# Optimization experiments

Measured on AMD Instinct MI355X. Metric: run time of the kernel, lower is better.

## Reference

```python
import jax, jax.numpy as jnp
import numpy as np

B, T, I, H, O = 128, 512, 512, 2048, 512

def setup_inputs() -> dict:
    key = jax.random.key(0)
    ks = jax.random.split(key, 10)
    s = lambda fan_in: 1.0 / np.sqrt(fan_in)
    return {
        "x": jax.random.normal(ks[0], (B, T, I), dtype=jnp.float32),
        "dt": jnp.zeros((1,), dtype=jnp.float32),            # torch init: Tensor([0])
        "a": jnp.ones((1,), dtype=jnp.float32),              # torch init: Tensor([1])
        "enc_w": jax.random.uniform(ks[1], (H, I), jnp.float32, -s(I), s(I)),
        "enc_b": jax.random.uniform(ks[2], (H,), jnp.float32, -s(I), s(I)),
        "rec_w": jax.random.uniform(ks[3], (H, H), jnp.float32, -s(H), s(H)),
        "rec_b": jax.random.uniform(ks[4], (H,), jnp.float32, -s(H), s(H)),
        "dec_w": jax.random.uniform(ks[5], (O, H), jnp.float32, -s(H), s(H)),
        "dec_b": jax.random.uniform(ks[6], (O,), jnp.float32, -s(H), s(H)),
        "hi_w": jax.random.uniform(ks[7], (H, 1), jnp.float32, -1.0, 1.0),
        "hi_b": jax.random.uniform(ks[8], (H,), jnp.float32, -1.0, 1.0),
    }

def reference(x, dt, a, enc_w, enc_b, rec_w, rec_b, dec_w, dec_b, hi_w, hi_b):
    # x: [B, T, I] -> time-major [T, B, I]
    xt = jnp.transpose(x, (1, 0, 2))
    sdt = jax.nn.sigmoid(dt[0])          # scalar gate
    av = a[0]
    # hidden_init(ones(B,1)) = hi_w[:,0] + hi_b, broadcast over batch
    h0 = jnp.broadcast_to(hi_w[:, 0] + hi_b, (x.shape[0], hi_b.shape[0]))
    # precompute encoder projection for all timesteps: [T, B, H]
    enc = jnp.einsum('tbi,hi->tbh', xt, enc_w) + enc_b

    def step(h, e_t):
        h = (1.0 - sdt) * h + sdt * jnp.tanh(e_t + av * (h @ rec_w.T + rec_b))
        y = h @ dec_w.T + dec_b
        return h, y

    hidden, output = jax.lax.scan(step, h0, enc)
    return output, hidden
```

## Files before the change

kernel.cpp:

```cpp
#include <hip/hip_runtime.h>
#include <hip/hip_bf16.h>
#include <cmath>

#define Bb 128
#define Tt 512
#define Ii 512
#define Hh 2048
#define Oo 512
#define REC_GRID 256

typedef __bf16 bf16_t;
typedef __bf16 bf16x8 __attribute__((ext_vector_type(8)));
typedef __bf16 bf16x4 __attribute__((ext_vector_type(4)));
typedef float  f32x4_t __attribute__((ext_vector_type(4)));
typedef unsigned u32;

static __device__ __forceinline__ bf16_t to_b(float v){ return (bf16_t)v; }
static __device__ __forceinline__ float  b2f(unsigned short u){ unsigned x = ((unsigned)u)<<16; return __builtin_bit_cast(float, x); }
static __device__ __forceinline__ unsigned short f2bbits(float v){ return __builtin_bit_cast(unsigned short, to_b(v)); }

static __device__ __forceinline__ void gl_lds16(const void* g, void* l){
  __builtin_amdgcn_global_load_lds((const __attribute__((address_space(1))) void*)g,
                                   (__attribute__((address_space(3))) void*)l, 16, 0, 0);
}

#define REP4(M) M(0)M(1)M(2)M(3)

__global__ __launch_bounds__(256) void k_f2b(bf16_t* __restrict__ dst, const float* __restrict__ src){
  size_t i = ((size_t)blockIdx.x*256 + threadIdx.x)*4;
  float4 v = *(const float4*)(src + i);
  bf16x4 o; o[0]=to_b(v.x); o[1]=to_b(v.y); o[2]=to_b(v.z); o[3]=to_b(v.w);
  *(bf16x4*)(dst + i) = o;
}

__global__ __launch_bounds__(256) void k_init_h0(const float* __restrict__ hi_w, const float* __restrict__ hi_b,
                                                 bf16_t* __restrict__ h0b){
  int i = blockIdx.x*256 + threadIdx.x;
  bf16_t vb = to_b(hi_w[i] + hi_b[i]);
  for (int b=0;b<Bb;++b) h0b[(size_t)b*Hh + i] = vb;
}

__global__ __launch_bounds__(256) void k_convert_x(const float* __restrict__ x, bf16_t* __restrict__ x_tm){
  size_t idx = ((size_t)blockIdx.x*256 + threadIdx.x)*8;
  int    i0  = (int)(idx % Ii);
  size_t m   = idx / Ii;
  int    t   = (int)(m / Bb), b = (int)(m % Bb);
  const float* s = x + ((size_t)b*Tt + t)*Ii + i0;
  float4 v0 = *(const float4*)s, v1 = *(const float4*)(s+4);
  bf16x8 o;
  o[0]=to_b(v0.x); o[1]=to_b(v0.y); o[2]=to_b(v0.z); o[3]=to_b(v0.w);
  o[4]=to_b(v1.x); o[5]=to_b(v1.y); o[6]=to_b(v1.z); o[7]=to_b(v1.w);
  *(bf16x8*)(x_tm + idx) = o;
}

template<int ROWS, int KB>
static __device__ __forceinline__ void stage(const bf16_t* __restrict__ g, long ld, long row0, int k0,
                                             char* __restrict__ ldsT){
  constexpr int SLOTS = KB/8;
  constexpr int PT    = ROWS*SLOTS/256;
  #pragma unroll
  for (int j=0;j<PT;++j){
    int c    = threadIdx.x + 256*j;
    int row  = c / SLOTS, slot = c % SLOTS;
    uint4 v  = *(const uint4*)(g + (row0+row)*ld + k0 + slot*8);
    *(uint4*)(ldsT + row*(KB*2) + ((slot*16) ^ ((row&7)<<4))) = v;
  }
}

template<int KB>
static __device__ __forceinline__ bf16x8 frag(const char* __restrict__ ldsT, int row, int kk, int lane){
  int kbyte = kk*64 + ((lane>>4)<<4);
  return *(const bf16x8*)(ldsT + row*(KB*2) + (kbyte ^ ((row&7)<<4)));
}

template<int EPI>
__global__ __launch_bounds__(256) void gemm128(const bf16_t* __restrict__ A, long lda,
                                               const bf16_t* __restrict__ Bw, long ldb,
                                               const float* __restrict__ bias,
                                               void* __restrict__ Cout, long ldc, int K){
  constexpr int TM=128, TN=128, KB=64;
  __shared__ char lds[(TM+TN)*KB*2];
  char* ldsA = lds;
  char* ldsB = lds + TM*KB*2;
  long m0 = (long)blockIdx.x * TM;
  long n0 = (long)blockIdx.y * TN;
  int w = threadIdx.x >> 6, lane = threadIdx.x & 63;
  int wm = w >> 1, wn = w & 1;
  f32x4_t acc[4][4] = {};
  for (int k0=0;k0<K;k0+=KB){
    __syncthreads();
    stage<TM,KB>(A,  lda, m0, k0, ldsA);
    stage<TN,KB>(Bw, ldb, n0, k0, ldsB);
    __syncthreads();
    #pragma unroll
    for (int kk=0;kk<KB/32;++kk){
      bf16x8 af[4], bfv[4];
      #pragma unroll
      for (int f=0;f<4;++f){ int r = wm*64 + f*16 + (lane&15); af[f]  = frag<KB>(ldsA, r, kk, lane); }
      #pragma unroll
      for (int f=0;f<4;++f){ int r = wn*64 + f*16 + (lane&15); bfv[f] = frag<KB>(ldsB, r, kk, lane); }
      #pragma unroll
      for (int i=0;i<4;++i)
        #pragma unroll
        for (int j=0;j<4;++j)
          acc[i][j] = __builtin_amdgcn_mfma_f32_16x16x32_bf16(af[i], bfv[j], acc[i][j], 0,0,0);
    }
  }
  #pragma unroll
  for (int i=0;i<4;++i)
    #pragma unroll
    for (int j=0;j<4;++j)
      #pragma unroll
      for (int e=0;e<4;++e){
        long row = m0 + wm*64 + i*16 + ((lane>>4)<<2) + e;
        long col = n0 + wn*64 + j*16 + (lane&15);
        float v = acc[i][j][e] + bias[col];
        if (EPI==0) ((bf16_t*)Cout)[row*ldc + col] = to_b(v);
        else        ((float*) Cout)[row*ldc + col] = v;
      }
}

__global__ __launch_bounds__(1024, 1) void rec_persist(
    const bf16_t* __restrict__ h0b, const bf16_t* __restrict__ W,
    bf16_t* __restrict__ EH, float* __restrict__ hfinal,
    const float* __restrict__ rec_b, const float* __restrict__ hi_w, const float* __restrict__ hi_b,
    const float* __restrict__ dtp, const float* __restrict__ ap,
    unsigned* __restrict__ flags)
{
  __shared__ char lds[65536 + 65536 + 4352];
  char*  hbuf = lds;
  float* redf = (float*)(lds + 65536);
  float* xbf  = (float*)(lds + 131072);

  const int bid = blockIdx.x;
  const int g   = bid & 7;
  const int n   = bid >> 3;
  const int m0  = g * 16;
  const int n0  = n * 64;
  unsigned* gflags = flags + g*32*16;
  const int tid = threadIdx.x, w = tid >> 6, lane = tid & 63;
  const int l15 = lane & 15, w4 = w*4;

  #define WDCL(i) bf16x8 wa##i, wb##i, wc##i, wd##i;
  REP4(WDCL)
  #undef WDCL
  #pragma unroll 1
  for (int p = 0; p < 2; ++p){
    __syncthreads();
    for (int it = 0; it < 8; ++it){
      int cid = it*1024 + tid;
      int lc  = cid & 63, kk = (cid >> 6) & 63, cgl = cid >> 12;
      uint4 v = *(const uint4*)(W + (size_t)(n0 + p*32 + cgl*16 + (lc&15))*Hh + kk*32 + ((lc>>4)<<3));
      *(uint4*)(lds + (size_t)cid*16) = v;
    }
    __syncthreads();
    if (p == 0){
      #define WRD(i) \
        wa##i = *(const bf16x8*)(lds + (size_t)((     w4 + (i))*64 + lane)*16); \
        wb##i = *(const bf16x8*)(lds + (size_t)((64 + w4 + (i))*64 + lane)*16);
      REP4(WRD)
      #undef WRD
    } else {
      #define WRD(i) \
        wc##i = *(const bf16x8*)(lds + (size_t)((     w4 + (i))*64 + lane)*16); \
        wd##i = *(const bf16x8*)(lds + (size_t)((64 + w4 + (i))*64 + lane)*16);
      REP4(WRD)
      #undef WRD
    }
  }
  __syncthreads();

  const float s  = 1.f/(1.f + __expf(-dtp[0]));
  const float av = ap[0];
  const int   cg_o = w & 3, eo = w >> 2;
  const int   batch = m0 + l15;
  const int   col_l = cg_o*16 + ((lane >> 4) << 2) + eo;
  const int   hcol  = n0 + col_l;
  const int   pos   = l15*65 + col_l;
  const float rbv = rec_b[hcol];
  float hm = hi_w[hcol] + hi_b[hcol];

  const size_t vsrc_off = (size_t)(m0 + l15)*Hh + ((lane>>4)<<3);
  const int co_b = m0 + (tid >> 5);
  const int co_c = n0 + (tid & 31)*2;
  const unsigned* fp = gflags + (w*2 + (lane & 1))*16;

  for (int t = 0; t < Tt; ++t){
    const bf16_t* Asrc = (t==0) ? h0b : (EH + (size_t)(t-1)*(Bb*Hh));
    bf16_t* EHt = EH + (size_t)t*(Bb*Hh);

    u32 ecv = 0;
    if (tid < 512)
      ecv = __hip_atomic_load((const u32*)(EHt + (size_t)co_b*Hh + co_c),
                              __ATOMIC_RELAXED, __HIP_MEMORY_SCOPE_AGENT);

    if (t){
      unsigned tt = (unsigned)t;
      for (;;){
        unsigned v = __hip_atomic_load(fp, __ATOMIC_RELAXED, __HIP_MEMORY_SCOPE_AGENT);
        if (__all((int)(v >= tt))) break;
        __builtin_amdgcn_s_sleep(2);
      }
    }

    {
      const bf16_t* src = Asrc + vsrc_off;
      #pragma unroll
      for (int i = 0; i < 4; ++i)
        gl_lds16(src + (w4 + i)*32, hbuf + (size_t)(w4 + i)*1024);
    }
    asm volatile("s_waitcnt vmcnt(0)" ::: "memory");

    f32x4_t acc0 = {0.f,0.f,0.f,0.f}, acc1 = acc0, acc2 = acc0, acc3 = acc0;
    #define KS(i) { \
      bf16x8 hv = *(const bf16x8*)(hbuf + (size_t)(w4 + (i))*1024 + (size_t)lane*16); \
      acc0 = __builtin_amdgcn_mfma_f32_16x16x32_bf16(wa##i, hv, acc0, 0,0,0); \
      acc1 = __builtin_amdgcn_mfma_f32_16x16x32_bf16(wb##i, hv, acc1, 0,0,0); \
      acc2 = __builtin_amdgcn_mfma_f32_16x16x32_bf16(wc##i, hv, acc2, 0,0,0); \
      acc3 = __builtin_amdgcn_mfma_f32_16x16x32_bf16(wd##i, hv, acc3, 0,0,0); }
    REP4(KS)
    #undef KS

    #pragma unroll
    for (int e=0;e<4;++e){
      redf[(w*16 +  0 + e)*64 + lane] = acc0[e];
      redf[(w*16 +  4 + e)*64 + lane] = acc1[e];
      redf[(w*16 +  8 + e)*64 + lane] = acc2[e];
      redf[(w*16 + 12 + e)*64 + lane] = acc3[e];
    }
    if (tid < 512){
      xbf[(tid>>5)*65 + (tid&31)*2    ] = b2f((unsigned short)(ecv & 0xffffu));
      xbf[(tid>>5)*65 + (tid&31)*2 + 1] = b2f((unsigned short)(ecv >> 16));
    }
    __syncthreads();

    float fa = 0.f;
    #pragma unroll
    for (int q=0;q<16;++q) fa += redf[(q*16 + cg_o*4 + eo)*64 + lane];

    {
      float enc = xbf[pos];
      float pre = enc + av*(fa + rbv);
      float th  = 1.f - 2.f/(__expf(2.f*pre) + 1.f);
      hm = (1.f - s)*hm + s*th;
      xbf[pos] = hm;
    }
    __syncthreads();

    if (tid < 512){
      float h0f = xbf[(tid>>5)*65 + (tid&31)*2];
      float h1f = xbf[(tid>>5)*65 + (tid&31)*2 + 1];
      u32 ov = (u32)f2bbits(h0f) | ((u32)f2bbits(h1f) << 16);
      __hip_atomic_store((u32*)(EHt + (size_t)co_b*Hh + co_c), ov,
                         __ATOMIC_RELAXED, __HIP_MEMORY_SCOPE_AGENT);
    }
    __syncthreads();
    if (tid == 0)
      __hip_atomic_store(gflags + n*16, (unsigned)(t+1),
                         __ATOMIC_RELAXED, __HIP_MEMORY_SCOPE_AGENT);
  }

  hfinal[(size_t)batch*Hh + hcol] = hm;
}

extern "C" void kernel_launch(void* const* d_in, const int* in_sizes, int n_in,
                              void* d_out, int out_size, void* d_ws, size_t ws_size,
                              hipStream_t stream){
  const float* x     = (const float*)d_in[0];
  const float* dt    = (const float*)d_in[1];
  const float* a     = (const float*)d_in[2];
  const float* enc_w = (const float*)d_in[3];
  const float* enc_b = (const float*)d_in[4];
  const float* rec_w = (const float*)d_in[5];
  const float* rec_b = (const float*)d_in[6];
  const float* dec_w = (const float*)d_in[7];
  const float* dec_b = (const float*)d_in[8];
  const float* hi_w  = (const float*)d_in[9];
  const float* hi_b  = (const float*)d_in[10];
  float* out = (float*)d_out;

  char* ws = (char*)d_ws;
  size_t off = 0;
  auto carve = [&](size_t bytes)->char*{ char* p = ws + off; off += (bytes + 255) & ~(size_t)255; return p; };
  bf16_t* x_tm   = (bf16_t*)carve((size_t)Tt*Bb*Ii*2);
  bf16_t* EH     = (bf16_t*)carve((size_t)Tt*Bb*Hh*2);
  bf16_t* h0b    = (bf16_t*)carve((size_t)Bb*Hh*2);
  bf16_t* enc_wb = (bf16_t*)carve((size_t)Hh*Ii*2);
  bf16_t* rec_wb = (bf16_t*)carve((size_t)Hh*Hh*2);
  bf16_t* dec_wb = (bf16_t*)carve((size_t)Oo*Hh*2);
  unsigned* flags = (unsigned*)carve(8*32*16*4);
  if (off > ws_size) return;

  hipMemsetAsync(flags, 0, 8*32*16*4, stream);

  k_f2b<<<(Hh*Ii)/1024, 256, 0, stream>>>(enc_wb, enc_w);
  k_f2b<<<(Hh*Hh)/1024, 256, 0, stream>>>(rec_wb, rec_w);
  k_f2b<<<(Oo*Hh)/1024, 256, 0, stream>>>(dec_wb, dec_w);
  k_init_h0<<<Hh/256, 256, 0, stream>>>(hi_w, hi_b, h0b);
  k_convert_x<<<((size_t)Tt*Bb*Ii/8)/256, 256, 0, stream>>>(x, x_tm);

  gemm128<0><<<dim3((Tt*Bb)/128, Hh/128), 256, 0, stream>>>(x_tm, Ii, enc_wb, Ii, enc_b, EH, Hh, Ii);

  {
    float* hfinal = out + (size_t)Tt*Bb*Oo;
    void* args[] = { (void*)&h0b, (void*)&rec_wb, (void*)&EH, (void*)&hfinal,
                     (void*)&rec_b, (void*)&hi_w, (void*)&hi_b, (void*)&dt, (void*)&a,
                     (void*)&flags };
    hipLaunchCooperativeKernel((const void*)rec_persist, dim3(REC_GRID), dim3(1024), args, 0, stream);
  }

  gemm128<1><<<dim3((Tt*Bb)/128, Oo/128), 256, 0, stream>>>(EH, Hh, dec_wb, Hh, dec_b, out, Oo, Hh);
}
```

Before: 2.406 ms.

## Split recurrent step into two batch halves with double-buffered h loads

Each block's 16 batch rows are split into two 8-row halves, each with its own set of progress flags and its own LDS buffer for h. While one half is being computed, the global-to-LDS load of the other half's previous hidden state is already in flight, so cross-block synchronisation latency overlaps with MFMA work. The waves are also re-partitioned to cover 8 k-chunks and 2 column groups each, with a two-stage LDS reduction in place of the old 16-way sum. In exchange, MFMAs still run over all 16 rows and only half the results are kept, so matrix work per step doubles. The change also adds more barriers and doubles the flag array.

```diff
diff --git a/kernel.cpp b/kernel.cpp
--- a/kernel.cpp
+++ b/kernel.cpp
@@ -24,7 +24,7 @@
                                    (__attribute__((address_space(3))) void*)l, 16, 0, 0);
 }
 
-#define REP4(M) M(0)M(1)M(2)M(3)
+#define REP8(M) M(0)M(1)M(2)M(3)M(4)M(5)M(6)M(7)
 
 __global__ __launch_bounds__(256) void k_f2b(bf16_t* __restrict__ dst, const float* __restrict__ src){
   size_t i = ((size_t)blockIdx.x*256 + threadIdx.x)*4;
@@ -127,44 +127,38 @@
     const float* __restrict__ dtp, const float* __restrict__ ap,
     unsigned* __restrict__ flags)
 {
-  __shared__ char lds[65536 + 65536 + 4352];
-  char*  hbuf = lds;
-  float* redf = (float*)(lds + 65536);
-  float* xbf  = (float*)(lds + 131072);
+  __shared__ char lds[65536 + 65536 + 16384 + 4352];
+  char*  hbufA = lds;
+  char*  hbufB = lds + 65536;
+  float* redf  = (float*)(lds + 131072);
+  float* xbf   = (float*)(lds + 147456);
 
   const int bid = blockIdx.x;
-  const int g   = bid & 7;
+  const int p   = bid & 7;
   const int n   = bid >> 3;
-  const int m0  = g * 16;
+  const int m0  = p * 16;
   const int n0  = n * 64;
-  unsigned* gflags = flags + g*32*16;
   const int tid = threadIdx.x, w = tid >> 6, lane = tid & 63;
   const int l15 = lane & 15, w4 = w*4;
-
-  #define WDCL(i) bf16x8 wa##i, wb##i, wc##i, wd##i;
-  REP4(WDCL)
-  #undef WDCL
+  const int ch = w & 1, ko = w >> 1, ko8 = ko*8;
+
+  bf16x8 wE0,wE1,wE2,wE3,wE4,wE5,wE6,wE7;
+  bf16x8 wO0,wO1,wO2,wO3,wO4,wO5,wO6,wO7;
   #pragma unroll 1
-  for (int p = 0; p < 2; ++p){
+  for (int p2 = 0; p2 < 2; ++p2){
     __syncthreads();
     for (int it = 0; it < 8; ++it){
       int cid = it*1024 + tid;
       int lc  = cid & 63, kk = (cid >> 6) & 63, cgl = cid >> 12;
-      uint4 v = *(const uint4*)(W + (size_t)(n0 + p*32 + cgl*16 + (lc&15))*Hh + kk*32 + ((lc>>4)<<3));
+      uint4 v = *(const uint4*)(W + (size_t)(n0 + p2*32 + cgl*16 + (lc&15))*Hh + kk*32 + ((lc>>4)<<3));
       *(uint4*)(lds + (size_t)cid*16) = v;
     }
     __syncthreads();
-    if (p == 0){
+    if (p2 == ch){
       #define WRD(i) \
-        wa##i = *(const bf16x8*)(lds + (size_t)((     w4 + (i))*64 + lane)*16); \
-        wb##i = *(const bf16x8*)(lds + (size_t)((64 + w4 + (i))*64 + lane)*16);
-      REP4(WRD)
-      #undef WRD
-    } else {
-      #define WRD(i) \
-        wc##i = *(const bf16x8*)(lds + (size_t)((     w4 + (i))*64 + lane)*16); \
-        wd##i = *(const bf16x8*)(lds + (size_t)((64 + w4 + (i))*64 + lane)*16);
-      REP4(WRD)
+        wE##i = *(const bf16x8*)(lds + (size_t)((     ko8 + (i))*64 + lane)*16); \
+        wO##i = *(const bf16x8*)(lds + (size_t)((64 + ko8 + (i))*64 + lane)*16);
+      REP8(WRD)
       #undef WRD
     }
   }
@@ -179,14 +173,28 @@
   const int   pos   = l15*65 + col_l;
   const float rbv = rec_b[hcol];
   float hm = hi_w[hcol] + hi_b[hcol];
+  const bool validA = (l15 < 8), validB = (l15 >= 8);
 
   const size_t vsrc_off = (size_t)(m0 + l15)*Hh + ((lane>>4)<<3);
   const int co_b = m0 + (tid >> 5);
   const int co_c = n0 + (tid & 31)*2;
-  const unsigned* fp = gflags + (w*2 + (lane & 1))*16;
+  const unsigned* fpA = flags + (((2*p  )*32) + ko*4 + (lane & 3))*16;
+  const unsigned* fpB = flags + (((2*p+1)*32) + ko*4 + (lane & 3))*16;
+  unsigned* flA = flags + ((2*p  )*32 + n)*16;
+  unsigned* flB = flags + ((2*p+1)*32 + n)*16;
+
+  auto volley = [&](const bf16_t* Asrc, char* hb){
+    const bf16_t* src = Asrc + vsrc_off;
+    #pragma unroll
+    for (int i = 0; i < 4; ++i)
+      gl_lds16(src + (w4 + i)*32, hb + (size_t)(w4 + i)*1024);
+  };
+
+  volley(h0b, hbufA);
+  __syncthreads();
 
   for (int t = 0; t < Tt; ++t){
-    const bf16_t* Asrc = (t==0) ? h0b : (EH + (size_t)(t-1)*(Bb*Hh));
+    const bf16_t* Aprev = (t==0) ? h0b : (EH + (size_t)(t-1)*(Bb*Hh));
     bf16_t* EHt = EH + (size_t)t*(Bb*Hh);
 
     u32 ecv = 0;
@@ -197,67 +205,131 @@
     if (t){
       unsigned tt = (unsigned)t;
       for (;;){
-        unsigned v = __hip_atomic_load(fp, __ATOMIC_RELAXED, __HIP_MEMORY_SCOPE_AGENT);
+        unsigned v = __hip_atomic_load(fpB, __ATOMIC_RELAXED, __HIP_MEMORY_SCOPE_AGENT);
         if (__all((int)(v >= tt))) break;
         __builtin_amdgcn_s_sleep(2);
       }
     }
+    volley(Aprev, hbufB);
 
     {
-      const bf16_t* src = Asrc + vsrc_off;
-      #pragma unroll
-      for (int i = 0; i < 4; ++i)
-        gl_lds16(src + (w4 + i)*32, hbuf + (size_t)(w4 + i)*1024);
-    }
-    asm volatile("s_waitcnt vmcnt(0)" ::: "memory");
-
-    f32x4_t acc0 = {0.f,0.f,0.f,0.f}, acc1 = acc0, acc2 = acc0, acc3 = acc0;
-    #define KS(i) { \
-      bf16x8 hv = *(const bf16x8*)(hbuf + (size_t)(w4 + (i))*1024 + (size_t)lane*16); \
-      acc0 = __builtin_amdgcn_mfma_f32_16x16x32_bf16(wa##i, hv, acc0, 0,0,0); \
-      acc1 = __builtin_amdgcn_mfma_f32_16x16x32_bf16(wb##i, hv, acc1, 0,0,0); \
-      acc2 = __builtin_amdgcn_mfma_f32_16x16x32_bf16(wc##i, hv, acc2, 0,0,0); \
-      acc3 = __builtin_amdgcn_mfma_f32_16x16x32_bf16(wd##i, hv, acc3, 0,0,0); }
-    REP4(KS)
-    #undef KS
-
-    #pragma unroll
-    for (int e=0;e<4;++e){
-      redf[(w*16 +  0 + e)*64 + lane] = acc0[e];
-      redf[(w*16 +  4 + e)*64 + lane] = acc1[e];
-      redf[(w*16 +  8 + e)*64 + lane] = acc2[e];
-      redf[(w*16 + 12 + e)*64 + lane] = acc3[e];
-    }
-    if (tid < 512){
-      xbf[(tid>>5)*65 + (tid&31)*2    ] = b2f((unsigned short)(ecv & 0xffffu));
-      xbf[(tid>>5)*65 + (tid&31)*2 + 1] = b2f((unsigned short)(ecv >> 16));
-    }
-    __syncthreads();
-
-    float fa = 0.f;
-    #pragma unroll
-    for (int q=0;q<16;++q) fa += redf[(q*16 + cg_o*4 + eo)*64 + lane];
+      f32x4_t aE = {0.f,0.f,0.f,0.f}, aO = aE;
+      #define KS(i) { \
+        bf16x8 hv = *(const bf16x8*)(hbufA + (size_t)(ko8 + (i))*1024 + (size_t)lane*16); \
+        aE = __builtin_amdgcn_mfma_f32_16x16x32_bf16(wE##i, hv, aE, 0,0,0); \
+        aO = __builtin_amdgcn_mfma_f32_16x16x32_bf16(wO##i, hv, aO, 0,0,0); }
+      REP8(KS)
+      #undef KS
+      if (ko >= 4){
+        #pragma unroll
+        for (int e=0;e<4;++e){
+          redf[(((ko-4)*4 + ch*2    )*4 + e)*64 + lane] = aE[e];
+          redf[(((ko-4)*4 + ch*2 + 1)*4 + e)*64 + lane] = aO[e];
+        }
+      }
+      if (tid < 256){
+        xbf[(tid>>5)*65 + (tid&31)*2    ] = b2f((unsigned short)(ecv & 0xffffu));
+        xbf[(tid>>5)*65 + (tid&31)*2 + 1] = b2f((unsigned short)(ecv >> 16));
+      }
+      __syncthreads();
+      if (ko < 4){
+        #pragma unroll
+        for (int e=0;e<4;++e){
+          aE[e] += redf[((ko*4 + ch*2    )*4 + e)*64 + lane];
+          aO[e] += redf[((ko*4 + ch*2 + 1)*4 + e)*64 + lane];
+        }
+        #pragma unroll
+        for (int e=0;e<4;++e){
+          redf[((ko*4 + ch*2    )*4 + e)*64 + lane] = aE[e];
+          redf[((ko*4 + ch*2 + 1)*4 + e)*64 + lane] = aO[e];
+        }
+      }
+      __syncthreads();
+      float fa = 0.f;
+      #pragma unroll
+      for (int kp=0;kp<4;++kp) fa += redf[((kp*4 + cg_o)*4 + eo)*64 + lane];
+      {
+        float enc = xbf[pos];
+        float pre = enc + av*(fa + rbv);
+        float th  = 1.f - 2.f/(__expf(2.f*pre) + 1.f);
+        if (validA){ hm = (1.f - s)*hm + s*th; xbf[pos] = hm; }
+      }
+      __syncthreads();
+      if (tid < 256){
+        float h0f = xbf[(tid>>5)*65 + (tid&31)*2];
+        float h1f = xbf[(tid>>5)*65 + (tid&31)*2 + 1];
+        u32 ov = (u32)f2bbits(h0f) | ((u32)f2bbits(h1f) << 16);
+        __hip_atomic_store((u32*)(EHt + (size_t)co_b*Hh + co_c), ov,
+                           __ATOMIC_RELAXED, __HIP_MEMORY_SCOPE_AGENT);
+      }
+      __syncthreads();
+      if (tid == 0)
+        __hip_atomic_store(flA, (unsigned)(t+1), __ATOMIC_RELAXED, __HIP_MEMORY_SCOPE_AGENT);
+    }
 
     {
-      float enc = xbf[pos];
-      float pre = enc + av*(fa + rbv);
-      float th  = 1.f - 2.f/(__expf(2.f*pre) + 1.f);
-      hm = (1.f - s)*hm + s*th;
-      xbf[pos] = hm;
-    }
-    __syncthreads();
-
-    if (tid < 512){
-      float h0f = xbf[(tid>>5)*65 + (tid&31)*2];
-      float h1f = xbf[(tid>>5)*65 + (tid&31)*2 + 1];
-      u32 ov = (u32)f2bbits(h0f) | ((u32)f2bbits(h1f) << 16);
-      __hip_atomic_store((u32*)(EHt + (size_t)co_b*Hh + co_c), ov,
-                         __ATOMIC_RELAXED, __HIP_MEMORY_SCOPE_AGENT);
-    }
-    __syncthreads();
-    if (tid == 0)
-      __hip_atomic_store(gflags + n*16, (unsigned)(t+1),
-                         __ATOMIC_RELAXED, __HIP_MEMORY_SCOPE_AGENT);
+      f32x4_t aE = {0.f,0.f,0.f,0.f}, aO = aE;
+      #define KS(i) { \
+        bf16x8 hv = *(const bf16x8*)(hbufB + (size_t)(ko8 + (i))*1024 + (size_t)lane*16); \
+        aE = __builtin_amdgcn_mfma_f32_16x16x32_bf16(wE##i, hv, aE, 0,0,0); \
+        aO = __builtin_amdgcn_mfma_f32_16x16x32_bf16(wO##i, hv, aO, 0,0,0); }
+      REP8(KS)
+      #undef KS
+      if (ko >= 4){
+        #pragma unroll
+        for (int e=0;e<4;++e){
+          redf[(((ko-4)*4 + ch*2    )*4 + e)*64 + lane] = aE[e];
+          redf[(((ko-4)*4 + ch*2 + 1)*4 + e)*64 + lane] = aO[e];
+        }
+      }
+      if (tid >= 256 && tid < 512){
+        xbf[(tid>>5)*65 + (tid&31)*2    ] = b2f((unsigned short)(ecv & 0xffffu));
+        xbf[(tid>>5)*65 + (tid&31)*2 + 1] = b2f((unsigned short)(ecv >> 16));
+      }
+      __syncthreads();
+      if (ko < 4){
+        #pragma unroll
+        for (int e=0;e<4;++e){
+          aE[e] += redf[((ko*4 + ch*2    )*4 + e)*64 + lane];
+          aO[e] += redf[((ko*4 + ch*2 + 1)*4 + e)*64 + lane];
+        }
+        #pragma unroll
+        for (int e=0;e<4;++e){
+          redf[((ko*4 + ch*2    )*4 + e)*64 + lane] = aE[e];
+          redf[((ko*4 + ch*2 + 1)*4 + e)*64 + lane] = aO[e];
+        }
+      }
+      __syncthreads();
+      float fa = 0.f;
+      #pragma unroll
+      for (int kp=0;kp<4;++kp) fa += redf[((kp*4 + cg_o)*4 + eo)*64 + lane];
+      {
+        float enc = xbf[pos];
+        float pre = enc + av*(fa + rbv);
+        float th  = 1.f - 2.f/(__expf(2.f*pre) + 1.f);
+        if (validB){ hm = (1.f - s)*hm + s*th; xbf[pos] = hm; }
+      }
+      __syncthreads();
+      if (tid >= 256 && tid < 512){
+        float h0f = xbf[(tid>>5)*65 + (tid&31)*2];
+        float h1f = xbf[(tid>>5)*65 + (tid&31)*2 + 1];
+        u32 ov = (u32)f2bbits(h0f) | ((u32)f2bbits(h1f) << 16);
+        __hip_atomic_store((u32*)(EHt + (size_t)co_b*Hh + co_c), ov,
+                           __ATOMIC_RELAXED, __HIP_MEMORY_SCOPE_AGENT);
+      }
+      if (t+1 < Tt){
+        unsigned tt = (unsigned)(t+1);
+        for (;;){
+          unsigned v = __hip_atomic_load(fpA, __ATOMIC_RELAXED, __HIP_MEMORY_SCOPE_AGENT);
+          if (__all((int)(v >= tt))) break;
+          __builtin_amdgcn_s_sleep(2);
+        }
+        volley(EHt, hbufA);
+      }
+      __syncthreads();
+      if (tid == 0)
+        __hip_atomic_store(flB, (unsigned)(t+1), __ATOMIC_RELAXED, __HIP_MEMORY_SCOPE_AGENT);
+    }
   }
 
   hfinal[(size_t)batch*Hh + hcol] = hm;
@@ -288,10 +360,10 @@
   bf16_t* enc_wb = (bf16_t*)carve((size_t)Hh*Ii*2);
   bf16_t* rec_wb = (bf16_t*)carve((size_t)Hh*Hh*2);
   bf16_t* dec_wb = (bf16_t*)carve((size_t)Oo*Hh*2);
-  unsigned* flags = (unsigned*)carve(8*32*16*4);
+  unsigned* flags = (unsigned*)carve(16*32*16*4);
   if (off > ws_size) return;
 
-  hipMemsetAsync(flags, 0, 8*32*16*4, stream);
+  hipMemsetAsync(flags, 0, 16*32*16*4, stream);
 
   k_f2b<<<(Hh*Ii)/1024, 256, 0, stream>>>(enc_wb, enc_w);
   k_f2b<<<(Hh*Hh)/1024, 256, 0, stream>>>(rec_wb, rec_w);
```

Measured after the change: 4.211 ms. +75.0%, slower.

## Use per-wave flags and fuse elementwise update to cut recurrent step barriers

Applied to the files above, without the earlier changes.

The recurrent step's epilogue is restructured so that 8 waves each compute two hidden columns directly from the reduced partial sums and write them to global memory, removing the xbf staging buffer and two block barriers. Each wave then publishes its own progress flag instead of one flag per block, and consumers poll per-wave flags before loading the next h slice into LDS at the end of the step. This shortens the critical path of the 512 serial steps. In exchange the flag array is larger and each consumer polls more flags, which adds polling traffic.

```diff
diff --git a/kernel.cpp b/kernel.cpp
--- a/kernel.cpp
+++ b/kernel.cpp
@@ -127,17 +127,16 @@
     const float* __restrict__ dtp, const float* __restrict__ ap,
     unsigned* __restrict__ flags)
 {
-  __shared__ char lds[65536 + 65536 + 4352];
+  __shared__ char lds[131072];
   char*  hbuf = lds;
   float* redf = (float*)(lds + 65536);
-  float* xbf  = (float*)(lds + 131072);
 
   const int bid = blockIdx.x;
   const int g   = bid & 7;
   const int n   = bid >> 3;
   const int m0  = g * 16;
   const int n0  = n * 64;
-  unsigned* gflags = flags + g*32*16;
+  unsigned* gflags = flags + g*256*16;
   const int tid = threadIdx.x, w = tid >> 6, lane = tid & 63;
   const int l15 = lane & 15, w4 = w*4;
 
@@ -172,44 +171,36 @@
 
   const float s  = 1.f/(1.f + __expf(-dtp[0]));
   const float av = ap[0];
-  const int   cg_o = w & 3, eo = w >> 2;
+  const int   cg_o = w & 3, ep = (w >> 2) & 1;
   const int   batch = m0 + l15;
-  const int   col_l = cg_o*16 + ((lane >> 4) << 2) + eo;
-  const int   hcol  = n0 + col_l;
-  const int   pos   = l15*65 + col_l;
-  const float rbv = rec_b[hcol];
-  float hm = hi_w[hcol] + hi_b[hcol];
+  const int   c0    = cg_o*16 + ((lane >> 4) << 2) + ep*2;
+  const size_t eoff = (size_t)batch*Hh + n0 + c0;
+  float rb0 = 0.f, rb1 = 0.f, hm0 = 0.f, hm1 = 0.f;
+  if (w < 8){
+    rb0 = rec_b[n0 + c0];     rb1 = rec_b[n0 + c0 + 1];
+    hm0 = hi_w[n0 + c0] + hi_b[n0 + c0];
+    hm1 = hi_w[n0 + c0 + 1] + hi_b[n0 + c0 + 1];
+  }
 
   const size_t vsrc_off = (size_t)(m0 + l15)*Hh + ((lane>>4)<<3);
-  const int co_b = m0 + (tid >> 5);
-  const int co_c = n0 + (tid & 31)*2;
-  const unsigned* fp = gflags + (w*2 + (lane & 1))*16;
+  const unsigned* fp = gflags + ((w*2 + ((lane>>3)&1))*8 + (lane&7))*16;
+  unsigned* myflag = gflags + (n*8 + w)*16;
+
+  {
+    const bf16_t* src = h0b + vsrc_off;
+    #pragma unroll
+    for (int i = 0; i < 4; ++i)
+      gl_lds16(src + (w4 + i)*32, hbuf + (size_t)(w4 + i)*1024);
+  }
+  asm volatile("s_waitcnt vmcnt(0)" ::: "memory");
 
   for (int t = 0; t < Tt; ++t){
-    const bf16_t* Asrc = (t==0) ? h0b : (EH + (size_t)(t-1)*(Bb*Hh));
     bf16_t* EHt = EH + (size_t)t*(Bb*Hh);
 
     u32 ecv = 0;
-    if (tid < 512)
-      ecv = __hip_atomic_load((const u32*)(EHt + (size_t)co_b*Hh + co_c),
+    if (w < 8)
+      ecv = __hip_atomic_load((const u32*)(EHt + eoff),
                               __ATOMIC_RELAXED, __HIP_MEMORY_SCOPE_AGENT);
-
-    if (t){
-      unsigned tt = (unsigned)t;
-      for (;;){
-        unsigned v = __hip_atomic_load(fp, __ATOMIC_RELAXED, __HIP_MEMORY_SCOPE_AGENT);
-        if (__all((int)(v >= tt))) break;
-        __builtin_amdgcn_s_sleep(2);
-      }
-    }
-
-    {
-      const bf16_t* src = Asrc + vsrc_off;
-      #pragma unroll
-      for (int i = 0; i < 4; ++i)
-        gl_lds16(src + (w4 + i)*32, hbuf + (size_t)(w4 + i)*1024);
-    }
-    asm volatile("s_waitcnt vmcnt(0)" ::: "memory");
 
     f32x4_t acc0 = {0.f,0.f,0.f,0.f}, acc1 = acc0, acc2 = acc0, acc3 = acc0;
     #define KS(i) { \
@@ -228,39 +219,51 @@
       redf[(w*16 +  8 + e)*64 + lane] = acc2[e];
       redf[(w*16 + 12 + e)*64 + lane] = acc3[e];
     }
-    if (tid < 512){
-      xbf[(tid>>5)*65 + (tid&31)*2    ] = b2f((unsigned short)(ecv & 0xffffu));
-      xbf[(tid>>5)*65 + (tid&31)*2 + 1] = b2f((unsigned short)(ecv >> 16));
-    }
-    __syncthreads();
-
-    float fa = 0.f;
-    #pragma unroll
-    for (int q=0;q<16;++q) fa += redf[(q*16 + cg_o*4 + eo)*64 + lane];
-
-    {
-      float enc = xbf[pos];
-      float pre = enc + av*(fa + rbv);
-      float th  = 1.f - 2.f/(__expf(2.f*pre) + 1.f);
-      hm = (1.f - s)*hm + s*th;
-      xbf[pos] = hm;
-    }
-    __syncthreads();
-
-    if (tid < 512){
-      float h0f = xbf[(tid>>5)*65 + (tid&31)*2];
-      float h1f = xbf[(tid>>5)*65 + (tid&31)*2 + 1];
-      u32 ov = (u32)f2bbits(h0f) | ((u32)f2bbits(h1f) << 16);
-      __hip_atomic_store((u32*)(EHt + (size_t)co_b*Hh + co_c), ov,
+    __syncthreads();
+
+    if (w < 8){
+      float fa0 = 0.f, fa1 = 0.f;
+      #pragma unroll
+      for (int q=0;q<16;++q){
+        fa0 += redf[(q*16 + cg_o*4 + ep*2    )*64 + lane];
+        fa1 += redf[(q*16 + cg_o*4 + ep*2 + 1)*64 + lane];
+      }
+      float enc0 = b2f((unsigned short)(ecv & 0xffffu));
+      float enc1 = b2f((unsigned short)(ecv >> 16));
+      float pre0 = enc0 + av*(fa0 + rb0);
+      float pre1 = enc1 + av*(fa1 + rb1);
+      float th0  = 1.f - 2.f/(__expf(2.f*pre0) + 1.f);
+      float th1  = 1.f - 2.f/(__expf(2.f*pre1) + 1.f);
+      hm0 = (1.f - s)*hm0 + s*th0;
+      hm1 = (1.f - s)*hm1 + s*th1;
+      u32 ov = (u32)f2bbits(hm0) | ((u32)f2bbits(hm1) << 16);
+      __hip_atomic_store((u32*)(EHt + eoff), ov,
                          __ATOMIC_RELAXED, __HIP_MEMORY_SCOPE_AGENT);
-    }
-    __syncthreads();
-    if (tid == 0)
-      __hip_atomic_store(gflags + n*16, (unsigned)(t+1),
-                         __ATOMIC_RELAXED, __HIP_MEMORY_SCOPE_AGENT);
-  }
-
-  hfinal[(size_t)batch*Hh + hcol] = hm;
+      asm volatile("s_waitcnt vmcnt(0)" ::: "memory");
+      if (lane == 0)
+        __hip_atomic_store(myflag, (unsigned)(t+1),
+                           __ATOMIC_RELAXED, __HIP_MEMORY_SCOPE_AGENT);
+    }
+
+    if (t+1 < Tt){
+      unsigned tt = (unsigned)(t+1);
+      for (;;){
+        unsigned v = __hip_atomic_load(fp, __ATOMIC_RELAXED, __HIP_MEMORY_SCOPE_AGENT);
+        if (__all((int)(v >= tt))) break;
+        __builtin_amdgcn_s_sleep(2);
+      }
+      const bf16_t* src = EHt + vsrc_off;
+      #pragma unroll
+      for (int i = 0; i < 4; ++i)
+        gl_lds16(src + (w4 + i)*32, hbuf + (size_t)(w4 + i)*1024);
+    }
+    __syncthreads();
+  }
+
+  if (w < 8){
+    float2 hv; hv.x = hm0; hv.y = hm1;
+    *(float2*)(hfinal + eoff) = hv;
+  }
 }
 
 extern "C" void kernel_launch(void* const* d_in, const int* in_sizes, int n_in,
@@ -288,10 +291,10 @@
   bf16_t* enc_wb = (bf16_t*)carve((size_t)Hh*Ii*2);
   bf16_t* rec_wb = (bf16_t*)carve((size_t)Hh*Hh*2);
   bf16_t* dec_wb = (bf16_t*)carve((size_t)Oo*Hh*2);
-  unsigned* flags = (unsigned*)carve(8*32*16*4);
+  unsigned* flags = (unsigned*)carve(8*256*16*4);
   if (off > ws_size) return;
 
-  hipMemsetAsync(flags, 0, 8*32*16*4, stream);
+  hipMemsetAsync(flags, 0, 8*256*16*4, stream);
 
   k_f2b<<<(Hh*Ii)/1024, 256, 0, stream>>>(enc_wb, enc_w);
   k_f2b<<<(Hh*Hh)/1024, 256, 0, stream>>>(rec_wb, rec_w);
```

Result: slower. 3.759 ms (+56.3%).
